# Optimization experiments

Hardware: AMD Instinct MI355X
Metric: run time of the kernel (lower is better)

Reference implementation:

```python
import jax, jax.numpy as jnp
import numpy as np

PS = 16          # patch_size
D = 768          # embed_dim (= conv_output_channels)
CIN = 8          # in_chans
HID = 128        # hypernet hidden width
WSIZE = D * PS * PS  # per-channel conv weight size (out=D, in=1, PSxPS)


def setup_inputs() -> dict:
    key = jax.random.key(0)
    ks = jax.random.split(key, 7)
    B, H, W = 32, 224, 224
    x = jax.random.normal(ks[0], (B, CIN, H, W), dtype=jnp.float32)
    channels = jax.random.randint(ks[1], (B, CIN), 0, CIN)
    # learned params; linears stored as [in, out] (math identical to torch x @ W.T + b)
    channel_embed = 0.02 * jax.random.normal(ks[2], (CIN, D), dtype=jnp.float32)
    fc1_w = jax.random.normal(ks[3], (D, HID), dtype=jnp.float32) / np.sqrt(D)
    fc1_b = jnp.zeros((HID,), dtype=jnp.float32)
    fc2_w = jax.random.normal(ks[4], (HID, WSIZE + D), dtype=jnp.float32) / np.sqrt(HID)
    fc2_b = jnp.zeros((WSIZE + D,), dtype=jnp.float32)
    return {"x": x, "channels": channels, "channel_embed": channel_embed,
            "fc1_w": fc1_w, "fc1_b": fc1_b, "fc2_w": fc2_w, "fc2_b": fc2_b}


def reference(x, channels, channel_embed, fc1_w, fc1_b, fc2_w, fc2_b):
    B, Cin, H, W = x.shape
    Hp, Wp = H // PS, W // PS
    # cur_channel_embed is computed in the original forward but never used
    _ = channel_embed[channels]
    # hypernetwork, batched over all channels (replaces the python loop)
    h = jax.nn.relu(channel_embed @ fc1_w + fc1_b)         # [Cin, 128]
    y = jnp.tanh(h @ fc2_w + fc2_b)                        # [Cin, WSIZE + D]
    wts = y[:, :WSIZE].reshape(Cin, D, PS, PS)             # per-channel conv kernels
    bias = y[:, WSIZE:]                                    # [Cin, D]
    # stride==kernel conv2d == non-overlapping patch matmul
    patches = x.reshape(B, Cin, Hp, PS, Wp, PS)
    out = jnp.einsum('bchpwq,cdpq->bchwd', patches, wts) + bias[None, :, None, None, :]
    # torch: stack(dim=2)->[B,D,Cin,Hp,Wp], flatten(2), transpose(1,2) => token order (c,h,w)
    return out.reshape(B, Cin * Hp * Wp, D)
```

## Files before the change

kernel.cpp:

```cpp
#include <hip/hip_runtime.h>
#include <hip/hip_bf16.h>

#define CIN 8
#define IMG 224
#define PS 16
#define HP 14
#define D_ 768
#define HID 128
#define MPT 196
#define K_ 256
#define WSIZE 196608
#define NJ 197376

typedef __bf16 bf16x8 __attribute__((ext_vector_type(8)));
typedef float f32x4 __attribute__((ext_vector_type(4)));

static __device__ __forceinline__ ushort f2bf(float f) {
  union { float f; unsigned int u; } x; x.f = f;
  unsigned int r = x.u + 0x7fffu + ((x.u >> 16) & 1u);
  return (ushort)(r >> 16);
}

static __device__ __forceinline__ void gload16(const void* g, void* l) {
  __builtin_amdgcn_global_load_lds(
      (const __attribute__((address_space(1))) unsigned int*)(uintptr_t)g,
      (__attribute__((address_space(3))) unsigned int*)(uintptr_t)l, 16, 0, 0);
}

__global__ __launch_bounds__(512) void k1_fc1(const float* __restrict__ ce,
                                              const float* __restrict__ w1,
                                              const float* __restrict__ b1,
                                              float* __restrict__ ht) {
  __shared__ float sh[3][HID];
  int c = blockIdx.x;
  int t = threadIdx.x;
  int i = t & 127, ksp = t >> 7;
  const float* cev = ce + c * D_ + ksp * 192;
  const float* wp = w1 + (size_t)(ksp * 192) * HID + i;
  float acc = 0.f;
#pragma unroll 8
  for (int d = 0; d < 192; ++d) acc = fmaf(cev[d], wp[(size_t)d * HID], acc);
  if (ksp) sh[ksp - 1][i] = acc;
  __syncthreads();
  if (ksp == 0) {
    float s = b1[i] + acc + sh[0][i] + sh[1][i] + sh[2][i];
    ht[i * CIN + c] = fmaxf(s, 0.f);
  }
}

__global__ __launch_bounds__(256) void k2_fc2(
    const float* __restrict__ ht, const float* __restrict__ w2,
    const float* __restrict__ b2, ushort* __restrict__ wbf,
    float* __restrict__ biasOut) {
  int t = threadIdx.x;
  int j = blockIdx.x * 256 + t;
  const float* wp = w2 + j;
  const float4* ht4 = (const float4*)ht;
  float4 a0 = {0, 0, 0, 0}, a1 = {0, 0, 0, 0};
#pragma unroll 8
  for (int i = 0; i < HID; ++i) {
    float wv = wp[(size_t)i * NJ];
    float4 hA = ht4[i * 2], hB = ht4[i * 2 + 1];
    a0.x = fmaf(hA.x, wv, a0.x); a0.y = fmaf(hA.y, wv, a0.y);
    a0.z = fmaf(hA.z, wv, a0.z); a0.w = fmaf(hA.w, wv, a0.w);
    a1.x = fmaf(hB.x, wv, a1.x); a1.y = fmaf(hB.y, wv, a1.y);
    a1.z = fmaf(hB.z, wv, a1.z); a1.w = fmaf(hB.w, wv, a1.w);
  }
  float bb = b2[j];
  if (j < WSIZE) {
    wbf[(size_t)0 * WSIZE + j] = f2bf(tanhf(a0.x + bb));
    wbf[(size_t)1 * WSIZE + j] = f2bf(tanhf(a0.y + bb));
    wbf[(size_t)2 * WSIZE + j] = f2bf(tanhf(a0.z + bb));
    wbf[(size_t)3 * WSIZE + j] = f2bf(tanhf(a0.w + bb));
    wbf[(size_t)4 * WSIZE + j] = f2bf(tanhf(a1.x + bb));
    wbf[(size_t)5 * WSIZE + j] = f2bf(tanhf(a1.y + bb));
    wbf[(size_t)6 * WSIZE + j] = f2bf(tanhf(a1.z + bb));
    wbf[(size_t)7 * WSIZE + j] = f2bf(tanhf(a1.w + bb));
  } else {
    int jb = j - WSIZE;
    biasOut[0 * D_ + jb] = tanhf(a0.x + bb);
    biasOut[1 * D_ + jb] = tanhf(a0.y + bb);
    biasOut[2 * D_ + jb] = tanhf(a0.z + bb);
    biasOut[3 * D_ + jb] = tanhf(a0.w + bb);
    biasOut[4 * D_ + jb] = tanhf(a1.x + bb);
    biasOut[5 * D_ + jb] = tanhf(a1.y + bb);
    biasOut[6 * D_ + jb] = tanhf(a1.z + bb);
    biasOut[7 * D_ + jb] = tanhf(a1.w + bb);
  }
}

__global__ __launch_bounds__(256, 3) void k3_gemm(
    const float* __restrict__ x, const ushort* __restrict__ wbf,
    const float* __restrict__ bias, float* __restrict__ out) {
  __shared__ float  As[2][128 * 32];
  __shared__ ushort Bs[2][128 * 32];

  int bid = blockIdx.x;
  int c = bid & 7;
  int rem = bid >> 3;
  int mt = rem / 6;
  int nt = rem - mt * 6;
  int m0 = mt * 128, n0 = nt * 128;

  int t = threadIdx.x;
  int lane = t & 63;
  int w = t >> 6;
  int wr = w >> 1, wc = w & 1;
  int rB = lane & 15;
  int h = lane >> 4;

  const ushort* wsrc = wbf + (size_t)c * WSIZE + (size_t)n0 * K_;

  int pA = (t & 7) ^ ((t >> 3) & 7);
  int prow = pA >> 2, qA = pA & 3;
  const float* asrc[4];
#pragma unroll
  for (int i = 0; i < 4; ++i) {
    int row = i * 32 + (t >> 3);
    int m = m0 + row;
    int b = m / MPT;
    int hw = m - b * MPT;
    int hp = hw / HP;
    int wp = hw - hp * HP;
    asrc[i] = x + ((size_t)(b * CIN + c) * IMG + hp * PS) * IMG + wp * PS
            + prow * IMG + qA * 4;
  }
  int pB = (t & 3) ^ ((t >> 2) & 3);
  const ushort* bsrc[2];
#pragma unroll
  for (int j = 0; j < 2; ++j)
    bsrc[j] = wsrc + ((t >> 2) + j * 64) * K_ + pB * 8;

#define K3_ISSUE(ks, buf)                                                    \
  {                                                                          \
    _Pragma("unroll") for (int i = 0; i < 4; ++i)                            \
        gload16(asrc[i] + (ks) * 2 * IMG, &As[buf][(i * 256 + w * 64) * 4]); \
    _Pragma("unroll") for (int j = 0; j < 2; ++j)                            \
        gload16(bsrc[j] + (ks) * 32, &Bs[buf][(j * 256 + w * 64) * 8]);      \
  }

  K3_ISSUE(0, 0);

  f32x4 acc[4][4] = {};

#pragma unroll
  for (int ks = 0; ks < 8; ++ks) {
    __syncthreads();
    if (ks < 7) K3_ISSUE(ks + 1, (ks + 1) & 1);
    const float*  Ab = As[ks & 1];
    const ushort* Bb = Bs[ks & 1];
    bf16x8 af[4], bq[4];
#pragma unroll
    for (int mi = 0; mi < 4; ++mi) {
      int r = wr * 64 + mi * 16 + rB;
      int s7 = r & 7;
      f32x4 lo = *(const f32x4*)&Ab[r * 32 + (((h * 2)     ^ s7) * 4)];
      f32x4 hi = *(const f32x4*)&Ab[r * 32 + (((h * 2 + 1) ^ s7) * 4)];
      union { __bf16 e[8]; bf16x8 v; } u;
      u.e[0] = (__bf16)lo[0]; u.e[1] = (__bf16)lo[1];
      u.e[2] = (__bf16)lo[2]; u.e[3] = (__bf16)lo[3];
      u.e[4] = (__bf16)hi[0]; u.e[5] = (__bf16)hi[1];
      u.e[6] = (__bf16)hi[2]; u.e[7] = (__bf16)hi[3];
      af[mi] = u.v;
    }
#pragma unroll
    for (int ni = 0; ni < 4; ++ni) {
      int r = wc * 64 + ni * 16 + rB;
      bq[ni] = *(const bf16x8*)&Bb[r * 32 + ((h ^ (r & 3)) * 8)];
    }
#pragma unroll
    for (int mi = 0; mi < 4; ++mi)
#pragma unroll
      for (int ni = 0; ni < 4; ++ni)
        acc[mi][ni] = __builtin_amdgcn_mfma_f32_16x16x32_bf16(af[mi], bq[ni], acc[mi][ni], 0, 0, 0);
  }

  float bv[4];
#pragma unroll
  for (int ni = 0; ni < 4; ++ni)
    bv[ni] = bias[c * D_ + n0 + wc * 64 + ni * 16 + rB];
#pragma unroll
  for (int mi = 0; mi < 4; ++mi) {
#pragma unroll
    for (int r = 0; r < 4; ++r) {
      int mrow = m0 + wr * 64 + mi * 16 + h * 4 + r;
      int b2 = mrow / MPT;
      int hw2 = mrow - b2 * MPT;
      float* op = out + ((size_t)b2 * (CIN * MPT) + c * MPT + hw2) * D_ + n0 + wc * 64 + rB;
#pragma unroll
      for (int ni = 0; ni < 4; ++ni)
        op[ni * 16] = acc[mi][ni][r] + bv[ni];
    }
  }
}

extern "C" void kernel_launch(void* const* d_in, const int* in_sizes, int n_in,
                              void* d_out, int out_size, void* d_ws, size_t ws_size,
                              hipStream_t stream) {
  const float* x  = (const float*)d_in[0];
  const float* ce = (const float*)d_in[2];
  const float* w1 = (const float*)d_in[3];
  const float* b1 = (const float*)d_in[4];
  const float* w2 = (const float*)d_in[5];
  const float* b2 = (const float*)d_in[6];
  float* out = (float*)d_out;

  char* ws = (char*)d_ws;
  float*  ht      = (float*)ws;
  float*  biasOut = (float*)(ws + 4096);
  ushort* wbf     = (ushort*)(ws + 4096 + 24576);

  k1_fc1<<<dim3(CIN), dim3(512), 0, stream>>>(ce, w1, b1, ht);
  k2_fc2<<<dim3(NJ / 256), dim3(256), 0, stream>>>(ht, w2, b2, wbf, biasOut);
  k3_gemm<<<dim3(8 * 49 * 6), dim3(256), 0, stream>>>(x, wbf, biasOut, out);
}
```

Before: 112.6 us.

## Pre-convert input to bf16 in fc2 kernel and simplify GEMM A-tile loads

Extra blocks appended to the fc2 kernel convert the whole fp32 input image to bf16 in workspace. The GEMM then loads bf16 A tiles directly, with a simpler k-split LDS layout and no per-iteration fp32-to-bf16 conversion. This halves the GEMM's A-operand traffic and LDS footprint, and occupancy is raised to 4 blocks per CU. In exchange it adds a full read and write pass over the input (about 51 MB read, 25 MB written) before the GEMM can start, and drops the XOR swizzle, which may cause LDS bank conflicts.

New measurement: 99.91 us. -11.3%, faster.

```diff
diff --git a/kernel.cpp b/kernel.cpp
--- a/kernel.cpp
+++ b/kernel.cpp
@@ -11,6 +11,7 @@
 #define K_ 256
 #define WSIZE 196608
 #define NJ 197376
+#define XN (32 * CIN * IMG * IMG)
 
 typedef __bf16 bf16x8 __attribute__((ext_vector_type(8)));
 typedef float f32x4 __attribute__((ext_vector_type(4)));
@@ -48,12 +49,27 @@
   }
 }
 
-__global__ __launch_bounds__(256) void k2_fc2(
+__global__ __launch_bounds__(256) void k2_fused(
     const float* __restrict__ ht, const float* __restrict__ w2,
-    const float* __restrict__ b2, ushort* __restrict__ wbf,
-    float* __restrict__ biasOut) {
+    const float* __restrict__ b2, const float* __restrict__ x,
+    ushort* __restrict__ wbf, float* __restrict__ biasOut,
+    ushort* __restrict__ xbf, int nCol) {
+  int bid = blockIdx.x;
   int t = threadIdx.x;
-  int j = blockIdx.x * 256 + t;
+  if (bid >= nCol) {
+    int u = (bid - nCol) * 256 + t;
+    int stride = (gridDim.x - nCol) * 256;
+    const float4* xv = (const float4*)x;
+    for (int v = u; v < XN / 8; v += stride) {
+      float4 f0 = xv[v * 2], f1 = xv[v * 2 + 1];
+      union { ushort s[8]; uint4 q; } pk;
+      pk.s[0] = f2bf(f0.x); pk.s[1] = f2bf(f0.y); pk.s[2] = f2bf(f0.z); pk.s[3] = f2bf(f0.w);
+      pk.s[4] = f2bf(f1.x); pk.s[5] = f2bf(f1.y); pk.s[6] = f2bf(f1.z); pk.s[7] = f2bf(f1.w);
+      *(uint4*)(xbf + (size_t)v * 8) = pk.q;
+    }
+    return;
+  }
+  int j = bid * 256 + t;
   const float* wp = w2 + j;
   const float4* ht4 = (const float4*)ht;
   float4 a0 = {0, 0, 0, 0}, a1 = {0, 0, 0, 0};
@@ -89,11 +105,11 @@
   }
 }
 
-__global__ __launch_bounds__(256, 3) void k3_gemm(
-    const float* __restrict__ x, const ushort* __restrict__ wbf,
+__global__ __launch_bounds__(256, 4) void k3_gemm(
+    const ushort* __restrict__ xbf, const ushort* __restrict__ wbf,
     const float* __restrict__ bias, float* __restrict__ out) {
-  __shared__ float  As[2][128 * 32];
-  __shared__ ushort Bs[2][128 * 32];
+  __shared__ ushort As[2][4096];
+  __shared__ ushort Bs[2][4096];
 
   int bid = blockIdx.x;
   int c = bid & 7;
@@ -109,34 +125,25 @@
   int rB = lane & 15;
   int h = lane >> 4;
 
-  const ushort* wsrc = wbf + (size_t)c * WSIZE + (size_t)n0 * K_;
-
-  int pA = (t & 7) ^ ((t >> 3) & 7);
-  int prow = pA >> 2, qA = pA & 3;
-  const float* asrc[4];
-#pragma unroll
-  for (int i = 0; i < 4; ++i) {
-    int row = i * 32 + (t >> 3);
-    int m = m0 + row;
+  int rowL = t & 127;
+  int p0 = t >> 7;
+  const ushort* aBase;
+  {
+    int m = m0 + rowL;
     int b = m / MPT;
     int hw = m - b * MPT;
     int hp = hw / HP;
     int wp = hw - hp * HP;
-    asrc[i] = x + ((size_t)(b * CIN + c) * IMG + hp * PS) * IMG + wp * PS
-            + prow * IMG + qA * 4;
-  }
-  int pB = (t & 3) ^ ((t >> 2) & 3);
-  const ushort* bsrc[2];
-#pragma unroll
-  for (int j = 0; j < 2; ++j)
-    bsrc[j] = wsrc + ((t >> 2) + j * 64) * K_ + pB * 8;
-
-#define K3_ISSUE(ks, buf)                                                    \
-  {                                                                          \
-    _Pragma("unroll") for (int i = 0; i < 4; ++i)                            \
-        gload16(asrc[i] + (ks) * 2 * IMG, &As[buf][(i * 256 + w * 64) * 4]); \
-    _Pragma("unroll") for (int j = 0; j < 2; ++j)                            \
-        gload16(bsrc[j] + (ks) * 32, &Bs[buf][(j * 256 + w * 64) * 8]);      \
+    aBase = xbf + ((size_t)(b * CIN + c) * IMG + hp * PS) * IMG + wp * PS + p0 * 8;
+  }
+  const ushort* bBase = wbf + (size_t)c * WSIZE + (size_t)(n0 + rowL) * K_ + p0 * 8;
+
+#define K3_ISSUE(ks, buf)                                               \
+  {                                                                     \
+    gload16(aBase + (ks) * 2 * IMG,       &As[buf][(w * 64) * 8]);      \
+    gload16(aBase + (ks) * 2 * IMG + IMG, &As[buf][(256 + w * 64) * 8]);\
+    gload16(bBase + (ks) * 32,            &Bs[buf][(w * 64) * 8]);      \
+    gload16(bBase + (ks) * 32 + 16,       &Bs[buf][(256 + w * 64) * 8]);\
   }
 
   K3_ISSUE(0, 0);
@@ -147,27 +154,15 @@
   for (int ks = 0; ks < 8; ++ks) {
     __syncthreads();
     if (ks < 7) K3_ISSUE(ks + 1, (ks + 1) & 1);
-    const float*  Ab = As[ks & 1];
+    const ushort* Ab = As[ks & 1];
     const ushort* Bb = Bs[ks & 1];
     bf16x8 af[4], bq[4];
 #pragma unroll
-    for (int mi = 0; mi < 4; ++mi) {
-      int r = wr * 64 + mi * 16 + rB;
-      int s7 = r & 7;
-      f32x4 lo = *(const f32x4*)&Ab[r * 32 + (((h * 2)     ^ s7) * 4)];
-      f32x4 hi = *(const f32x4*)&Ab[r * 32 + (((h * 2 + 1) ^ s7) * 4)];
-      union { __bf16 e[8]; bf16x8 v; } u;
-      u.e[0] = (__bf16)lo[0]; u.e[1] = (__bf16)lo[1];
-      u.e[2] = (__bf16)lo[2]; u.e[3] = (__bf16)lo[3];
-      u.e[4] = (__bf16)hi[0]; u.e[5] = (__bf16)hi[1];
-      u.e[6] = (__bf16)hi[2]; u.e[7] = (__bf16)hi[3];
-      af[mi] = u.v;
-    }
-#pragma unroll
-    for (int ni = 0; ni < 4; ++ni) {
-      int r = wc * 64 + ni * 16 + rB;
-      bq[ni] = *(const bf16x8*)&Bb[r * 32 + ((h ^ (r & 3)) * 8)];
-    }
+    for (int mi = 0; mi < 4; ++mi)
+      af[mi] = *(const bf16x8*)&Ab[h * 1024 + (wr * 64 + mi * 16 + rB) * 8];
+#pragma unroll
+    for (int ni = 0; ni < 4; ++ni)
+      bq[ni] = *(const bf16x8*)&Bb[h * 1024 + (wc * 64 + ni * 16 + rB) * 8];
 #pragma unroll
     for (int mi = 0; mi < 4; ++mi)
 #pragma unroll
@@ -209,8 +204,12 @@
   float*  ht      = (float*)ws;
   float*  biasOut = (float*)(ws + 4096);
   ushort* wbf     = (ushort*)(ws + 4096 + 24576);
+  ushort* xbf     = (ushort*)(ws + 4096 + 24576 + 3145728);
+
+  int nCol = NJ / 256;
+  int nConv = 512;
 
   k1_fc1<<<dim3(CIN), dim3(512), 0, stream>>>(ce, w1, b1, ht);
-  k2_fc2<<<dim3(NJ / 256), dim3(256), 0, stream>>>(ht, w2, b2, wbf, biasOut);
-  k3_gemm<<<dim3(8 * 49 * 6), dim3(256), 0, stream>>>(x, wbf, biasOut, out);
-}
+  k2_fused<<<dim3(nCol + nConv), dim3(256), 0, stream>>>(ht, w2, b2, x, wbf, biasOut, xbf, nCol);
+  k3_gemm<<<dim3(8 * 49 * 6), dim3(256), 0, stream>>>(xbf, wbf, biasOut, out);
+}
```

## Triple-buffer GEMM LDS with manual waitcnt and k-major LDS layout

Applied to the files above, without the earlier changes.

Moves the patch GEMM from double to triple buffering, so loads run two k-steps ahead, and replaces __syncthreads with explicit vmcnt waits plus s_barrier. The LDS staging becomes k-chunk-major (each thread loads one row across two k-chunks) instead of XOR-swizzled rows, which changes both the global access pattern and the LDS read addressing. The larger LDS footprint lowers the occupancy hint from 3 to 2 blocks per CU. The hand-written waitcnt values assume exact load counts, and the new layout may cause LDS bank conflicts.

Result: slower. 128.4 us (+14.0%).

```diff
diff --git a/kernel.cpp b/kernel.cpp
--- a/kernel.cpp
+++ b/kernel.cpp
@@ -89,11 +89,11 @@
   }
 }
 
-__global__ __launch_bounds__(256, 3) void k3_gemm(
+__global__ __launch_bounds__(256, 2) void k3_gemm(
     const float* __restrict__ x, const ushort* __restrict__ wbf,
     const float* __restrict__ bias, float* __restrict__ out) {
-  __shared__ float  As[2][128 * 32];
-  __shared__ ushort Bs[2][128 * 32];
+  __shared__ float  As[3][4096];
+  __shared__ ushort Bs[3][4096];
 
   int bid = blockIdx.x;
   int c = bid & 7;
@@ -109,53 +109,49 @@
   int rB = lane & 15;
   int h = lane >> 4;
 
-  const ushort* wsrc = wbf + (size_t)c * WSIZE + (size_t)n0 * K_;
-
-  int pA = (t & 7) ^ ((t >> 3) & 7);
-  int prow = pA >> 2, qA = pA & 3;
-  const float* asrc[4];
-#pragma unroll
-  for (int i = 0; i < 4; ++i) {
-    int row = i * 32 + (t >> 3);
-    int m = m0 + row;
+  int rowL = t & 127, p0 = t >> 7;
+
+  const float* aBase;
+  {
+    int m = m0 + rowL;
     int b = m / MPT;
     int hw = m - b * MPT;
     int hp = hw / HP;
     int wp = hw - hp * HP;
-    asrc[i] = x + ((size_t)(b * CIN + c) * IMG + hp * PS) * IMG + wp * PS
-            + prow * IMG + qA * 4;
-  }
-  int pB = (t & 3) ^ ((t >> 2) & 3);
-  const ushort* bsrc[2];
-#pragma unroll
-  for (int j = 0; j < 2; ++j)
-    bsrc[j] = wsrc + ((t >> 2) + j * 64) * K_ + pB * 8;
-
-#define K3_ISSUE(ks, buf)                                                    \
-  {                                                                          \
-    _Pragma("unroll") for (int i = 0; i < 4; ++i)                            \
-        gload16(asrc[i] + (ks) * 2 * IMG, &As[buf][(i * 256 + w * 64) * 4]); \
-    _Pragma("unroll") for (int j = 0; j < 2; ++j)                            \
-        gload16(bsrc[j] + (ks) * 32, &Bs[buf][(j * 256 + w * 64) * 8]);      \
+    aBase = x + ((size_t)(b * CIN + c) * IMG + hp * PS) * IMG + wp * PS + p0 * 4;
+  }
+  const ushort* bBase = wbf + (size_t)c * WSIZE + (size_t)(n0 + rowL) * K_ + p0 * 8;
+
+#define K3_ISSUE(ks, buf)                                                     \
+  {                                                                           \
+    const float* a_ = aBase + (ks) * 2 * IMG;                                 \
+    gload16(a_,            &As[buf][(0 * 256 + w * 64) * 4]);                 \
+    gload16(a_ + 8,        &As[buf][(1 * 256 + w * 64) * 4]);                 \
+    gload16(a_ + IMG,      &As[buf][(2 * 256 + w * 64) * 4]);                 \
+    gload16(a_ + IMG + 8,  &As[buf][(3 * 256 + w * 64) * 4]);                 \
+    gload16(bBase + (ks) * 32,       &Bs[buf][(0 * 256 + w * 64) * 8]);       \
+    gload16(bBase + (ks) * 32 + 16,  &Bs[buf][(1 * 256 + w * 64) * 8]);       \
   }
 
   K3_ISSUE(0, 0);
+  K3_ISSUE(1, 1);
 
   f32x4 acc[4][4] = {};
 
 #pragma unroll
   for (int ks = 0; ks < 8; ++ks) {
-    __syncthreads();
-    if (ks < 7) K3_ISSUE(ks + 1, (ks + 1) & 1);
-    const float*  Ab = As[ks & 1];
-    const ushort* Bb = Bs[ks & 1];
+    if (ks < 7) asm volatile("s_waitcnt vmcnt(6) lgkmcnt(0)" ::: "memory");
+    else        asm volatile("s_waitcnt vmcnt(0) lgkmcnt(0)" ::: "memory");
+    __builtin_amdgcn_s_barrier();
+    if (ks < 6) K3_ISSUE(ks + 2, (ks + 2) % 3);
+    const float*  Af = As[ks % 3];
+    const ushort* Bf = Bs[ks % 3];
     bf16x8 af[4], bq[4];
 #pragma unroll
     for (int mi = 0; mi < 4; ++mi) {
       int r = wr * 64 + mi * 16 + rB;
-      int s7 = r & 7;
-      f32x4 lo = *(const f32x4*)&Ab[r * 32 + (((h * 2)     ^ s7) * 4)];
-      f32x4 hi = *(const f32x4*)&Ab[r * 32 + (((h * 2 + 1) ^ s7) * 4)];
+      f32x4 lo = *(const f32x4*)&Af[(2 * h) * 512 + r * 4];
+      f32x4 hi = *(const f32x4*)&Af[(2 * h + 1) * 512 + r * 4];
       union { __bf16 e[8]; bf16x8 v; } u;
       u.e[0] = (__bf16)lo[0]; u.e[1] = (__bf16)lo[1];
       u.e[2] = (__bf16)lo[2]; u.e[3] = (__bf16)lo[3];
@@ -164,10 +160,8 @@
       af[mi] = u.v;
     }
 #pragma unroll
-    for (int ni = 0; ni < 4; ++ni) {
-      int r = wc * 64 + ni * 16 + rB;
-      bq[ni] = *(const bf16x8*)&Bb[r * 32 + ((h ^ (r & 3)) * 8)];
-    }
+    for (int ni = 0; ni < 4; ++ni)
+      bq[ni] = *(const bf16x8*)&Bf[h * 1024 + (wc * 64 + ni * 16 + rB) * 8];
 #pragma unroll
     for (int mi = 0; mi < 4; ++mi)
 #pragma unroll
```
